# Performance work log

Measured on AMD Instinct MI355X. Metric: run time of the kernel, lower is better.

Reference implementation:

```python
import math
import jax, jax.numpy as jnp
import numpy as np

DIM = 1024
N_HEADS = 16
HEAD_DIM = DIM // N_HEADS
MAX_SEQ_LEN = 4096
ROPE_BASE = 10000.0


def _rope_tables(seq_len):
    # [S, head_dim//2] cos/sin tables, matching RotaryPositionalEncoding buffers
    inv_freq = 1.0 / (ROPE_BASE ** (jnp.arange(0, HEAD_DIM, 2, dtype=jnp.float32) / HEAD_DIM))
    t = jnp.arange(seq_len, dtype=jnp.float32)
    freqs = jnp.outer(t, inv_freq)
    return jnp.cos(freqs), jnp.sin(freqs)


def _rotate_half(x):
    # interleaved rotate: out[..., 0::2] = -x[..., 1::2]; out[..., 1::2] = x[..., 0::2]
    x1 = x[..., 0::2]
    x2 = x[..., 1::2]
    return jnp.stack([-x2, x1], axis=-1).reshape(x.shape)


def _apply_rope(xq, xk, cos, sin):
    # cos/sin: [S, head_dim//2] -> repeat_interleave(2) -> [1, 1, S, head_dim]
    cos = jnp.repeat(cos, 2, axis=-1)[None, None]
    sin = jnp.repeat(sin, 2, axis=-1)[None, None]
    xq_out = xq * cos + _rotate_half(xq) * sin
    xk_out = xk * cos + _rotate_half(xk) * sin
    return xq_out, xk_out


def setup_inputs() -> dict:
    key = jax.random.key(0)
    kx, kq, kk, kv, ko = jax.random.split(key, 5)
    B, S = 1, 4096
    x = jax.random.normal(kx, (B, S, DIM), dtype=jnp.float32)
    scale = 0.02
    Wq = jax.random.normal(kq, (DIM, DIM), dtype=jnp.float32) * scale
    Wk = jax.random.normal(kk, (DIM, DIM), dtype=jnp.float32) * scale
    Wv = jax.random.normal(kv, (DIM, DIM), dtype=jnp.float32) * scale
    Wo = jax.random.normal(ko, (DIM, DIM), dtype=jnp.float32) * scale
    return {"x": x, "Wq": Wq, "Wk": Wk, "Wv": Wv, "Wo": Wo}


def reference(x, Wq, Wk, Wv, Wo):
    B, S, _ = x.shape
    # torch nn.Linear: y = x @ W.T
    q = (x @ Wq.T).reshape(B, S, N_HEADS, HEAD_DIM).transpose(0, 2, 1, 3)  # [B,H,S,D]
    k = (x @ Wk.T).reshape(B, S, N_HEADS, HEAD_DIM).transpose(0, 2, 1, 3)
    v = (x @ Wv.T).reshape(B, S, N_HEADS, HEAD_DIM).transpose(0, 2, 1, 3)

    cos, sin = _rope_tables(S)  # start_pos = 0
    q, k = _apply_rope(q, k, cos, sin)

    scores = jnp.einsum('bhqd,bhkd->bhqk', q, k) / math.sqrt(HEAD_DIM)
    # causal mask (start_pos=0, no KV cache): upper triangle above diag gets -inf
    mask = jnp.triu(jnp.full((S, S), -jnp.inf, dtype=scores.dtype), k=1)
    scores = scores + mask[None, None]
    probs = jax.nn.softmax(scores, axis=-1)
    out = jnp.einsum('bhqk,bhkd->bhqd', probs, v)  # [B,H,S,D]
    out = out.transpose(0, 2, 1, 3).reshape(B, S, DIM)
    return out @ Wo.T
```

## Files before the change

### kernel.cpp

```cpp
#include <hip/hip_runtime.h>


typedef __attribute__((ext_vector_type(4))) float f32x4;
typedef __attribute__((ext_vector_type(8))) short short8;
typedef __attribute__((ext_vector_type(2))) unsigned int u32x2;
typedef unsigned short u16;

#define SEQ 4096
#define DIMM 1024
#define NH 16
#define HD 64

__device__ __forceinline__ u16 f2b(float f) {
  unsigned u = __float_as_uint(f);
  u += 0x7FFFu + ((u >> 16) & 1u);
  return (u16)(u >> 16);
}
__device__ __forceinline__ f32x4 mfma16(short8 a, short8 b, f32x4 c) {
  return __builtin_amdgcn_mfma_f32_16x16x32_bf16(a, b, c, 0, 0, 0);
}
#define GLL16(gp, lp)                                                        \
  __builtin_amdgcn_global_load_lds(                                          \
      (const __attribute__((address_space(1))) unsigned int*)(gp),           \
      (__attribute__((address_space(3))) unsigned int*)(lp), 16, 0, 0)

__global__ __launch_bounds__(256) void cvt_all(
    const float* __restrict__ x, const float* __restrict__ wq,
    const float* __restrict__ wk, const float* __restrict__ wv,
    const float* __restrict__ wo,
    u16* __restrict__ xb, u16* __restrict__ wqb, u16* __restrict__ wkb,
    u16* __restrict__ wvb, u16* __restrict__ wob, float2* __restrict__ tab) {
  int i = blockIdx.x * 256 + threadIdx.x;
  if (i < 2097152) {
    const float* src;
    u16* dst;
    int j;
    if (i < 1048576) {
      src = x; dst = xb; j = i;
    } else {
      int t = i - 1048576;
      int wsel = t >> 18;
      j = t & 262143;
      src = (wsel == 0) ? wq : (wsel == 1) ? wk : (wsel == 2) ? wv : wo;
      dst = (wsel == 0) ? wqb : (wsel == 1) ? wkb : (wsel == 2) ? wvb : wob;
    }
    float4 v = ((const float4*)src)[j];
    ushort4 o;
    o.x = f2b(v.x); o.y = f2b(v.y); o.z = f2b(v.z); o.w = f2b(v.w);
    ((ushort4*)dst)[j] = o;
  } else {
    int j = i - 2097152;
    int s = j >> 6, d = j & 63, fi = d >> 1;
    float ang = (float)s * powf(10000.0f, -(float)fi * (1.0f / 32.0f));
    float sn, cs;
    sincosf(ang, &sn, &cs);
    tab[j] = make_float2(cs, (d & 1) ? sn : -sn);
  }
}

template <int MODE>
__global__ __launch_bounds__(256) void gemm_bt(
    const u16* __restrict__ A, const u16* __restrict__ B, float* __restrict__ C,
    const float2* __restrict__ tab, u16* __restrict__ Qh, u16* __restrict__ Kh,
    u16* __restrict__ Vh, int K, int N) {
  __shared__ __align__(16) u16 As[2][4096];
  __shared__ __align__(16) u16 Bs[2][4096];
  const int tid = threadIdx.x;
  const int bm = blockIdx.x, bn = blockIdx.y;
  const int w = tid >> 6, lane = tid & 63;
  const int wm = w >> 1, wn = w & 1;
  const int l15 = lane & 15, g = lane >> 4;

  f32x4 acc[4][4] = {};

  const u16* Ap0 = A + (size_t)(bm * 128 + (tid >> 2)) * K + (tid & 3) * 8;
  const u16* Ap1 = Ap0 + (size_t)64 * K;
  const u16* Bp0 = B + (size_t)(bn * 128 + (tid >> 2)) * K + (tid & 3) * 8;
  const u16* Bp1 = Bp0 + (size_t)64 * K;

  GLL16(Ap0, &As[0][w * 512]);
  GLL16(Ap1, &As[0][2048 + w * 512]);
  GLL16(Bp0, &Bs[0][w * 512]);
  GLL16(Bp1, &Bs[0][2048 + w * 512]);
  __syncthreads();

  const int nk = K >> 5;
  for (int t = 0; t < nk; ++t) {
    const int cur = t & 1;
    if (t + 1 < nk) {
      const int k1 = (t + 1) * 32;
      GLL16(Ap0 + k1, &As[cur ^ 1][w * 512]);
      GLL16(Ap1 + k1, &As[cur ^ 1][2048 + w * 512]);
      GLL16(Bp0 + k1, &Bs[cur ^ 1][w * 512]);
      GLL16(Bp1 + k1, &Bs[cur ^ 1][2048 + w * 512]);
    }
    short8 af[4], bf[4];
#pragma unroll
    for (int m = 0; m < 4; ++m)
      af[m] = *(const short8*)&As[cur][(wm * 64 + m * 16 + l15) * 32 + g * 8];
#pragma unroll
    for (int n = 0; n < 4; ++n)
      bf[n] = *(const short8*)&Bs[cur][(wn * 64 + n * 16 + l15) * 32 + g * 8];
#pragma unroll
    for (int m = 0; m < 4; ++m)
#pragma unroll
      for (int n = 0; n < 4; ++n)
        acc[m][n] = mfma16(af[m], bf[n], acc[m][n]);
    __syncthreads();
  }

  if (MODE == 0) {
#pragma unroll
    for (int m = 0; m < 4; ++m) {
      int grow = bm * 128 + wm * 64 + m * 16 + g * 4;
#pragma unroll
      for (int n = 0; n < 4; ++n) {
        int gcol = bn * 128 + wn * 64 + n * 16 + l15;
#pragma unroll
        for (int r = 0; r < 4; ++r)
          C[(size_t)(grow + r) * N + gcol] = acc[m][n][r];
      }
    }
  } else {
    const int sector = bn >> 3;
    const int hh = (bn & 7) * 2 + wn;
    u16* dst = (sector == 0) ? Qh : (sector == 1) ? Kh : Vh;
    const float qs = (sector == 0) ? 0.125f : 1.0f;
#pragma unroll
    for (int m = 0; m < 4; ++m) {
#pragma unroll
      for (int n = 0; n < 4; ++n) {
        const int d = n * 16 + l15;
#pragma unroll
        for (int r = 0; r < 4; ++r) {
          const int srow = bm * 128 + wm * 64 + m * 16 + g * 4 + r;
          float v = acc[m][n][r];
          float val;
          if (sector < 2) {
            float p = __shfl_xor(v, 1);
            float2 tc = tab[srow * 64 + d];
            val = (v * tc.x + p * tc.y) * qs;
          } else {
            val = v;
          }
          float valn = __shfl_xor(val, 1);
          if (!(l15 & 1)) {
            unsigned pk;
            asm("v_cvt_pk_bf16_f32 %0, %1, %2" : "=v"(pk) : "v"(val), "v"(valn));
            *(unsigned*)&dst[((size_t)hh * SEQ + srow) * HD + d] = pk;
          }
        }
      }
    }
  }
}

__global__ __launch_bounds__(256, 4) void attn_fwd(
    const u16* __restrict__ Qh, const u16* __restrict__ Kh,
    const u16* __restrict__ Vh, u16* __restrict__ Ob) {
  __shared__ __align__(16) u16 Ks[2][64 * 64];
  __shared__ __align__(16) u16 Vt[2][64 * 64];
  __shared__ __align__(16) u16 Ps[4][16 * 64];

  const int L = blockIdx.x;
  const int xcd = L & 7, sl = L >> 3;
  const int h = xcd + 8 * (sl >> 6);
  const int cp = sl & 63;
  const int c = (cp < 32) ? (63 - 2 * cp) : (2 * (cp - 32));

  const int tid = threadIdx.x, w = tid >> 6, lane = tid & 63;
  const int l15 = lane & 15, g = lane >> 4;
  const int qr0 = c * 64 + w * 16;
  const size_t hS = (size_t)h * SEQ;

  const int krow0 = w * 8 + (lane >> 3);
  const int kc0 = ((lane & 7) ^ (krow0 & 7)) * 8;
  const int krow1 = 32 + krow0;
  const int kc1 = ((lane & 7) ^ (krow1 & 7)) * 8;
  const int kvp = tid >> 3, d0 = (tid & 7) * 8;
  const u16* Vsrc = Vh + (hS + kvp * 2) * HD + d0;
  int voff[8];
#pragma unroll
  for (int j = 0; j < 8; ++j) {
    int d = d0 + j;
    int sw = (d ^ (d >> 3)) & 7;
    voff[j] = d * 64 + (((kvp >> 2) ^ sw) << 3) + (kvp & 3) * 2;
  }

  const u16* Qp = Qh + (hS + qr0 + l15) * HD + g * 8;
  short8 qf0 = *(const short8*)(Qp);
  short8 qf1 = *(const short8*)(Qp + 32);

  f32x4 o[4] = {};
  float m_ = -3.0e38f, lg = 0.f;

  GLL16(Kh + (hS + krow0) * HD + kc0, &Ks[0][w * 512]);
  GLL16(Kh + (hS + krow1) * HD + kc1, &Ks[0][2048 + w * 512]);
  short8 va = *(const short8*)(Vsrc);
  short8 vb = *(const short8*)(Vsrc + HD);

  for (int t = 0; t <= c; ++t) {
    const int cur = t & 1;
    {
      u16* vtb = &Vt[cur][0];
#pragma unroll
      for (int j = 0; j < 8; ++j) {
        ushort2 pr;
        pr.x = (u16)va[j];
        pr.y = (u16)vb[j];
        *(ushort2*)(vtb + voff[j]) = pr;
      }
    }
    __syncthreads();
    if (t < c) {
      const size_t kb_ = hS + (size_t)(t + 1) * 64;
      GLL16(Kh + (kb_ + krow0) * HD + kc0, &Ks[cur ^ 1][w * 512]);
      GLL16(Kh + (kb_ + krow1) * HD + kc1, &Ks[cur ^ 1][2048 + w * 512]);
      va = *(const short8*)(Vsrc + (size_t)(t + 1) * 64 * HD);
      vb = *(const short8*)(Vsrc + (size_t)(t + 1) * 64 * HD + HD);
    }
    f32x4 s[4] = {};
#pragma unroll
    for (int kb = 0; kb < 4; ++kb) {
      int row = kb * 16 + l15;
      short8 k0 = *(const short8*)&Ks[cur][row * 64 + ((g ^ (row & 7)) << 3)];
      short8 k1 = *(const short8*)&Ks[cur][row * 64 + (((4 + g) ^ (row & 7)) << 3)];
      s[kb] = mfma16(k0, qf0, s[kb]);
      s[kb] = mfma16(k1, qf1, s[kb]);
    }
    if (t == c) {
      const int kv0 = t * 64;
      int q = qr0 + l15;
#pragma unroll
      for (int kb = 0; kb < 4; ++kb) {
        int kvb = kv0 + kb * 16 + g * 4;
#pragma unroll
        for (int r = 0; r < 4; ++r)
          if (kvb + r > q) s[kb][r] = -1.0e30f;
      }
    }
    float mx = fmaxf(fmaxf(fmaxf(s[0][0], s[0][1]), fmaxf(s[0][2], s[0][3])),
                     fmaxf(fmaxf(fmaxf(s[1][0], s[1][1]), fmaxf(s[1][2], s[1][3])),
                           fmaxf(fmaxf(fmaxf(s[2][0], s[2][1]), fmaxf(s[2][2], s[2][3])),
                                 fmaxf(fmaxf(s[3][0], s[3][1]), fmaxf(s[3][2], s[3][3])))));
    mx = fmaxf(mx, __shfl_xor(mx, 16));
    mx = fmaxf(mx, __shfl_xor(mx, 32));
    if (!__all(mx - m_ <= 8.0f)) {
      float nm = fmaxf(m_, mx);
      float sc = __expf(m_ - nm);
      m_ = nm;
      lg *= sc;
#pragma unroll
      for (int r = 0; r < 4; ++r) {
        float so = __shfl(sc, g * 4 + r);
        o[0][r] *= so; o[1][r] *= so; o[2][r] *= so; o[3][r] *= so;
      }
    }
    {
      float ps = 0.f;
#pragma unroll
      for (int kb = 0; kb < 4; ++kb) {
        float p0 = __expf(s[kb][0] - m_);
        float p1 = __expf(s[kb][1] - m_);
        float p2 = __expf(s[kb][2] - m_);
        float p3 = __expf(s[kb][3] - m_);
        ps += (p0 + p1) + (p2 + p3);
        unsigned w0, w1;
        asm("v_cvt_pk_bf16_f32 %0, %1, %2" : "=v"(w0) : "v"(p0), "v"(p1));
        asm("v_cvt_pk_bf16_f32 %0, %1, %2" : "=v"(w1) : "v"(p2), "v"(p3));
        int ch = (kb * 2 + (g >> 1)) ^ (l15 & 7);
        *(u32x2*)&Ps[w][l15 * 64 + ch * 8 + (g & 1) * 4] = (u32x2){w0, w1};
      }
      lg += ps;
    }
    short8 pa0 = *(const short8*)&Ps[w][l15 * 64 + ((g ^ (l15 & 7)) << 3)];
    short8 pa1 = *(const short8*)&Ps[w][l15 * 64 + (((4 + g) ^ (l15 & 7)) << 3)];
#pragma unroll
    for (int nb = 0; nb < 4; ++nb) {
      int rv = nb * 16 + l15;
      int swv = (rv ^ (rv >> 3)) & 7;
      short8 v0f = *(const short8*)&Vt[cur][rv * 64 + ((g ^ swv) << 3)];
      short8 v1f = *(const short8*)&Vt[cur][rv * 64 + (((4 + g) ^ swv) << 3)];
      o[nb] = mfma16(pa0, v0f, o[nb]);
      o[nb] = mfma16(pa1, v1f, o[nb]);
    }
  }

  float l = lg;
  l += __shfl_xor(l, 16);
  l += __shfl_xor(l, 32);
  float il = 1.0f / l;
#pragma unroll
  for (int r = 0; r < 4; ++r) {
    float ilr = __shfl(il, g * 4 + r);
    int qrow = qr0 + g * 4 + r;
#pragma unroll
    for (int nb = 0; nb < 4; ++nb)
      Ob[(size_t)qrow * DIMM + h * HD + nb * 16 + l15] = f2b(o[nb][r] * ilr);
  }
}

#define OFF_XB 0u
#define OFF_WQKV 8388608u
#define OFF_WOB 14680064u
#define OFF_TAB 16777216u
#define OFF_QH 18874368u
#define OFF_KH 27262976u
#define OFF_VH 35651584u
#define OFF_OB 44040192u

extern "C" void kernel_launch(void* const* d_in, const int* in_sizes, int n_in,
                              void* d_out, int out_size, void* d_ws, size_t ws_size,
                              hipStream_t stream) {
  const float* x = (const float*)d_in[0];
  const float* Wq = (const float*)d_in[1];
  const float* Wk = (const float*)d_in[2];
  const float* Wv = (const float*)d_in[3];
  const float* Wo = (const float*)d_in[4];
  float* out = (float*)d_out;
  char* ws = (char*)d_ws;

  u16* xb = (u16*)(ws + OFF_XB);
  u16* wqkv = (u16*)(ws + OFF_WQKV);
  u16* wqb = wqkv;
  u16* wkb = wqkv + (size_t)DIMM * DIMM;
  u16* wvb = wqkv + (size_t)2 * DIMM * DIMM;
  u16* wob = (u16*)(ws + OFF_WOB);
  float2* tab = (float2*)(ws + OFF_TAB);
  u16* Qh = (u16*)(ws + OFF_QH);
  u16* Kh = (u16*)(ws + OFF_KH);
  u16* Vh = (u16*)(ws + OFF_VH);
  u16* Ob = (u16*)(ws + OFF_OB);

  cvt_all<<<9216, 256, 0, stream>>>(x, Wq, Wk, Wv, Wo, xb, wqb, wkb, wvb, wob, tab);

  gemm_bt<1><<<dim3(SEQ / 128, 3072 / 128), 256, 0, stream>>>(
      xb, wqkv, nullptr, tab, Qh, Kh, Vh, DIMM, 3072);

  attn_fwd<<<1024, 256, 0, stream>>>(Qh, Kh, Vh, Ob);

  gemm_bt<0><<<dim3(SEQ / 128, DIMM / 128), 256, 0, stream>>>(
      Ob, wob, out, nullptr, nullptr, nullptr, nullptr, DIMM, DIMM);
}
```

Baseline: 257.9 us.

## Triple-buffer GEMM loads, simplify attention block mapping, raise MFMA priority

The GEMM moves from a double- to a triple-buffered LDS pipeline with two tiles in flight. It uses explicit vmcnt waits and a single barrier per iteration instead of two __syncthreads. The attention kernel drops the XCD-aware head/chunk interleaving for a simple longest-first mapping. It also wraps the QK and PV MFMA sections in s_setprio to favour matrix work across waves. Triple buffering raises GEMM LDS use, which may reduce occupancy, and the new block order may lose L2 locality per XCD.

```diff
diff --git a/kernel.cpp b/kernel.cpp
--- a/kernel.cpp
+++ b/kernel.cpp
@@ -63,8 +63,8 @@
     const u16* __restrict__ A, const u16* __restrict__ B, float* __restrict__ C,
     const float2* __restrict__ tab, u16* __restrict__ Qh, u16* __restrict__ Kh,
     u16* __restrict__ Vh, int K, int N) {
-  __shared__ __align__(16) u16 As[2][4096];
-  __shared__ __align__(16) u16 Bs[2][4096];
+  __shared__ __align__(16) u16 As[3][4096];
+  __shared__ __align__(16) u16 Bs[3][4096];
   const int tid = threadIdx.x;
   const int bm = blockIdx.x, bn = blockIdx.y;
   const int w = tid >> 6, lane = tid & 63;
@@ -82,17 +82,27 @@
   GLL16(Ap1, &As[0][2048 + w * 512]);
   GLL16(Bp0, &Bs[0][w * 512]);
   GLL16(Bp1, &Bs[0][2048 + w * 512]);
-  __syncthreads();
+  GLL16(Ap0 + 32, &As[1][w * 512]);
+  GLL16(Ap1 + 32, &As[1][2048 + w * 512]);
+  GLL16(Bp0 + 32, &Bs[1][w * 512]);
+  GLL16(Bp1 + 32, &Bs[1][2048 + w * 512]);
 
   const int nk = K >> 5;
+  int cur = 0;
   for (int t = 0; t < nk; ++t) {
-    const int cur = t & 1;
-    if (t + 1 < nk) {
-      const int k1 = (t + 1) * 32;
-      GLL16(Ap0 + k1, &As[cur ^ 1][w * 512]);
-      GLL16(Ap1 + k1, &As[cur ^ 1][2048 + w * 512]);
-      GLL16(Bp0 + k1, &Bs[cur ^ 1][w * 512]);
-      GLL16(Bp1 + k1, &Bs[cur ^ 1][2048 + w * 512]);
+    if (t + 1 < nk)
+      asm volatile("s_waitcnt vmcnt(4)" ::: "memory");
+    else
+      asm volatile("s_waitcnt vmcnt(0)" ::: "memory");
+    __builtin_amdgcn_s_barrier();
+    asm volatile("" ::: "memory");
+    if (t + 2 < nk) {
+      const int k2 = (t + 2) * 32;
+      const int nb = (t + 2) % 3;
+      GLL16(Ap0 + k2, &As[nb][w * 512]);
+      GLL16(Ap1 + k2, &As[nb][2048 + w * 512]);
+      GLL16(Bp0 + k2, &Bs[nb][w * 512]);
+      GLL16(Bp1 + k2, &Bs[nb][2048 + w * 512]);
     }
     short8 af[4], bf[4];
 #pragma unroll
@@ -106,7 +116,7 @@
 #pragma unroll
       for (int n = 0; n < 4; ++n)
         acc[m][n] = mfma16(af[m], bf[n], acc[m][n]);
-    __syncthreads();
+    cur = (cur == 2) ? 0 : cur + 1;
   }
 
   if (MODE == 0) {
@@ -163,10 +173,8 @@
   __shared__ __align__(16) u16 Ps[4][16 * 64];
 
   const int L = blockIdx.x;
-  const int xcd = L & 7, sl = L >> 3;
-  const int h = xcd + 8 * (sl >> 6);
-  const int cp = sl & 63;
-  const int c = (cp < 32) ? (63 - 2 * cp) : (2 * (cp - 32));
+  const int h = L & 15;
+  const int c = 63 - (L >> 4);
 
   const int tid = threadIdx.x, w = tid >> 6, lane = tid & 63;
   const int l15 = lane & 15, g = lane >> 4;
@@ -220,6 +228,7 @@
       vb = *(const short8*)(Vsrc + (size_t)(t + 1) * 64 * HD + HD);
     }
     f32x4 s[4] = {};
+    __builtin_amdgcn_s_setprio(1);
 #pragma unroll
     for (int kb = 0; kb < 4; ++kb) {
       int row = kb * 16 + l15;
@@ -228,6 +237,7 @@
       s[kb] = mfma16(k0, qf0, s[kb]);
       s[kb] = mfma16(k1, qf1, s[kb]);
     }
+    __builtin_amdgcn_s_setprio(0);
     if (t == c) {
       const int kv0 = t * 64;
       int q = qr0 + l15;
@@ -275,6 +285,7 @@
     }
     short8 pa0 = *(const short8*)&Ps[w][l15 * 64 + ((g ^ (l15 & 7)) << 3)];
     short8 pa1 = *(const short8*)&Ps[w][l15 * 64 + (((4 + g) ^ (l15 & 7)) << 3)];
+    __builtin_amdgcn_s_setprio(1);
 #pragma unroll
     for (int nb = 0; nb < 4; ++nb) {
       int rv = nb * 16 + l15;
@@ -284,6 +295,7 @@
       o[nb] = mfma16(pa0, v0f, o[nb]);
       o[nb] = mfma16(pa1, v1f, o[nb]);
     }
+    __builtin_amdgcn_s_setprio(0);
   }
 
   float l = lg;
```

Result: no change. 257.2 us (-0.3%).

## Split long causal attention rows across two blocks and merge partials

Applied to the files above, without the earlier changes.

Query tiles whose causal range is 32 or more KV tiles are now split into two halves processed by separate blocks. Each half writes unnormalized fp32 partial outputs plus its running max and sum, and a new merge kernel combines them. The change also narrows the output projection tile to 128x64 for more blocks, adds setprio around the MFMA sections, and packs the QKV epilogue stores so every lane writes. The aim is to cut load imbalance and the long tail from the heaviest causal tiles, at the cost of an extra kernel launch and added fp32 partial traffic.

```diff
diff --git a/kernel.cpp b/kernel.cpp
--- a/kernel.cpp
+++ b/kernel.cpp
@@ -58,11 +58,11 @@
   }
 }
 
-template <int MODE>
-__global__ __launch_bounds__(256) void gemm_bt(
-    const u16* __restrict__ A, const u16* __restrict__ B, float* __restrict__ C,
+__global__ __launch_bounds__(256) void gemm_qkv(
+    const u16* __restrict__ A, const u16* __restrict__ B,
     const float2* __restrict__ tab, u16* __restrict__ Qh, u16* __restrict__ Kh,
-    u16* __restrict__ Vh, int K, int N) {
+    u16* __restrict__ Vh) {
+  const int K = DIMM;
   __shared__ __align__(16) u16 As[2][4096];
   __shared__ __align__(16) u16 Bs[2][4096];
   const int tid = threadIdx.x;
@@ -109,64 +109,136 @@
     __syncthreads();
   }
 
-  if (MODE == 0) {
-#pragma unroll
-    for (int m = 0; m < 4; ++m) {
-      int grow = bm * 128 + wm * 64 + m * 16 + g * 4;
-#pragma unroll
-      for (int n = 0; n < 4; ++n) {
-        int gcol = bn * 128 + wn * 64 + n * 16 + l15;
-#pragma unroll
-        for (int r = 0; r < 4; ++r)
-          C[(size_t)(grow + r) * N + gcol] = acc[m][n][r];
-      }
-    }
-  } else {
-    const int sector = bn >> 3;
-    const int hh = (bn & 7) * 2 + wn;
-    u16* dst = (sector == 0) ? Qh : (sector == 1) ? Kh : Vh;
-    const float qs = (sector == 0) ? 0.125f : 1.0f;
-#pragma unroll
-    for (int m = 0; m < 4; ++m) {
-#pragma unroll
-      for (int n = 0; n < 4; ++n) {
-        const int d = n * 16 + l15;
-#pragma unroll
-        for (int r = 0; r < 4; ++r) {
-          const int srow = bm * 128 + wm * 64 + m * 16 + g * 4 + r;
-          float v = acc[m][n][r];
-          float val;
-          if (sector < 2) {
-            float p = __shfl_xor(v, 1);
-            float2 tc = tab[srow * 64 + d];
-            val = (v * tc.x + p * tc.y) * qs;
-          } else {
-            val = v;
-          }
-          float valn = __shfl_xor(val, 1);
-          if (!(l15 & 1)) {
-            unsigned pk;
-            asm("v_cvt_pk_bf16_f32 %0, %1, %2" : "=v"(pk) : "v"(val), "v"(valn));
-            *(unsigned*)&dst[((size_t)hh * SEQ + srow) * HD + d] = pk;
-          }
+  const int sector = bn >> 3;
+  const int hh = (bn & 7) * 2 + wn;
+  u16* dst = (sector == 0) ? Qh : (sector == 1) ? Kh : Vh;
+  const float qs = (sector == 0) ? 0.125f : 1.0f;
+  const int evenlane = !(l15 & 1);
+  const int dd0 = (l15 & ~1);
+#pragma unroll
+  for (int m = 0; m < 4; ++m) {
+    const int sb = bm * 128 + wm * 64 + m * 16 + g * 4;
+#pragma unroll
+    for (int n = 0; n < 4; ++n) {
+      const int d = n * 16 + l15;
+      float val[4];
+#pragma unroll
+      for (int r = 0; r < 4; ++r) {
+        float v = acc[m][n][r];
+        if (sector < 2) {
+          float p = __shfl_xor(v, 1);
+          float2 tc = tab[(sb + r) * 64 + d];
+          val[r] = (v * tc.x + p * tc.y) * qs;
+        } else {
+          val[r] = v;
         }
       }
+      float x0 = __shfl_xor(val[0], 1);
+      float x1 = __shfl_xor(val[1], 1);
+      float x2 = __shfl_xor(val[2], 1);
+      float x3 = __shfl_xor(val[3], 1);
+      float aLo = evenlane ? val[0] : x2;
+      float aHi = evenlane ? x0 : val[2];
+      float bLo = evenlane ? val[1] : x3;
+      float bHi = evenlane ? x1 : val[3];
+      unsigned pkA, pkB;
+      asm("v_cvt_pk_bf16_f32 %0, %1, %2" : "=v"(pkA) : "v"(aLo), "v"(aHi));
+      asm("v_cvt_pk_bf16_f32 %0, %1, %2" : "=v"(pkB) : "v"(bLo), "v"(bHi));
+      const int rA = evenlane ? 0 : 2, rB = evenlane ? 1 : 3;
+      const int dcol = n * 16 + dd0;
+      *(unsigned*)&dst[((size_t)hh * SEQ + sb + rA) * HD + dcol] = pkA;
+      *(unsigned*)&dst[((size_t)hh * SEQ + sb + rB) * HD + dcol] = pkB;
+    }
+  }
+}
+
+__global__ __launch_bounds__(256) void gemm_o(
+    const u16* __restrict__ A, const u16* __restrict__ B, float* __restrict__ C) {
+  const int K = DIMM;
+  __shared__ __align__(16) u16 As[2][4096];
+  __shared__ __align__(16) u16 Bs[2][2048];
+  const int tid = threadIdx.x;
+  const int bm = blockIdx.x, bn = blockIdx.y;
+  const int w = tid >> 6, lane = tid & 63;
+  const int wm = w >> 1, wn = w & 1;
+  const int l15 = lane & 15, g = lane >> 4;
+
+  f32x4 acc[4][2] = {};
+
+  const u16* Ap0 = A + (size_t)(bm * 128 + (tid >> 2)) * K + (tid & 3) * 8;
+  const u16* Ap1 = Ap0 + (size_t)64 * K;
+  const u16* Bp0 = B + (size_t)(bn * 64 + (tid >> 2)) * K + (tid & 3) * 8;
+
+  GLL16(Ap0, &As[0][w * 512]);
+  GLL16(Ap1, &As[0][2048 + w * 512]);
+  GLL16(Bp0, &Bs[0][w * 512]);
+  __syncthreads();
+
+  const int nk = K >> 5;
+  for (int t = 0; t < nk; ++t) {
+    const int cur = t & 1;
+    if (t + 1 < nk) {
+      const int k1 = (t + 1) * 32;
+      GLL16(Ap0 + k1, &As[cur ^ 1][w * 512]);
+      GLL16(Ap1 + k1, &As[cur ^ 1][2048 + w * 512]);
+      GLL16(Bp0 + k1, &Bs[cur ^ 1][w * 512]);
+    }
+    short8 af[4], bf[2];
+#pragma unroll
+    for (int m = 0; m < 4; ++m)
+      af[m] = *(const short8*)&As[cur][(wm * 64 + m * 16 + l15) * 32 + g * 8];
+#pragma unroll
+    for (int n = 0; n < 2; ++n)
+      bf[n] = *(const short8*)&Bs[cur][(wn * 32 + n * 16 + l15) * 32 + g * 8];
+#pragma unroll
+    for (int m = 0; m < 4; ++m)
+#pragma unroll
+      for (int n = 0; n < 2; ++n)
+        acc[m][n] = mfma16(af[m], bf[n], acc[m][n]);
+    __syncthreads();
+  }
+
+#pragma unroll
+  for (int m = 0; m < 4; ++m) {
+    int grow = bm * 128 + wm * 64 + m * 16 + g * 4;
+#pragma unroll
+    for (int n = 0; n < 2; ++n) {
+      int gcol = bn * 64 + wn * 32 + n * 16 + l15;
+#pragma unroll
+      for (int r = 0; r < 4; ++r)
+        C[(size_t)(grow + r) * DIMM + gcol] = acc[m][n][r];
     }
   }
 }
 
 __global__ __launch_bounds__(256, 4) void attn_fwd(
     const u16* __restrict__ Qh, const u16* __restrict__ Kh,
-    const u16* __restrict__ Vh, u16* __restrict__ Ob) {
+    const u16* __restrict__ Vh, u16* __restrict__ Ob,
+    float* __restrict__ Opart, float2* __restrict__ ml) {
   __shared__ __align__(16) u16 Ks[2][64 * 64];
   __shared__ __align__(16) u16 Vt[2][64 * 64];
   __shared__ __align__(16) u16 Ps[4][16 * 64];
 
   const int L = blockIdx.x;
-  const int xcd = L & 7, sl = L >> 3;
-  const int h = xcd + 8 * (sl >> 6);
-  const int cp = sl & 63;
-  const int c = (cp < 32) ? (63 - 2 * cp) : (2 * (cp - 32));
+  const int h = L & 15;
+  const int u = L >> 4;
+  int c, t0, t1, half = 0;
+  if (u < 80) {
+    int i = u / 5, j = u % 5;
+    if (j < 4) {
+      c = 63 - 2 * i - (j >> 1);
+      half = j & 1;
+      int mid = (c + 2) >> 1;
+      t0 = half ? mid : 0;
+      t1 = half ? (c + 1) : mid;
+    } else {
+      c = 31 - i; t0 = 0; t1 = c + 1;
+    }
+  } else {
+    c = 15 - (u - 80); t0 = 0; t1 = c + 1;
+  }
+  const int heavy = (c >= 32);
+  const int nt = t1 - t0;
 
   const int tid = threadIdx.x, w = tid >> 6, lane = tid & 63;
   const int l15 = lane & 15, g = lane >> 4;
@@ -194,13 +266,14 @@
   f32x4 o[4] = {};
   float m_ = -3.0e38f, lg = 0.f;
 
-  GLL16(Kh + (hS + krow0) * HD + kc0, &Ks[0][w * 512]);
-  GLL16(Kh + (hS + krow1) * HD + kc1, &Ks[0][2048 + w * 512]);
-  short8 va = *(const short8*)(Vsrc);
-  short8 vb = *(const short8*)(Vsrc + HD);
-
-  for (int t = 0; t <= c; ++t) {
-    const int cur = t & 1;
+  GLL16(Kh + (hS + (size_t)t0 * 64 + krow0) * HD + kc0, &Ks[0][w * 512]);
+  GLL16(Kh + (hS + (size_t)t0 * 64 + krow1) * HD + kc1, &Ks[0][2048 + w * 512]);
+  short8 va = *(const short8*)(Vsrc + (size_t)t0 * 64 * HD);
+  short8 vb = *(const short8*)(Vsrc + (size_t)t0 * 64 * HD + HD);
+
+  for (int tt = 0; tt < nt; ++tt) {
+    const int t = t0 + tt;
+    const int cur = tt & 1;
     {
       u16* vtb = &Vt[cur][0];
 #pragma unroll
@@ -212,7 +285,7 @@
       }
     }
     __syncthreads();
-    if (t < c) {
+    if (tt + 1 < nt) {
       const size_t kb_ = hS + (size_t)(t + 1) * 64;
       GLL16(Kh + (kb_ + krow0) * HD + kc0, &Ks[cur ^ 1][w * 512]);
       GLL16(Kh + (kb_ + krow1) * HD + kc1, &Ks[cur ^ 1][2048 + w * 512]);
@@ -220,6 +293,7 @@
       vb = *(const short8*)(Vsrc + (size_t)(t + 1) * 64 * HD + HD);
     }
     f32x4 s[4] = {};
+    __builtin_amdgcn_s_setprio(1);
 #pragma unroll
     for (int kb = 0; kb < 4; ++kb) {
       int row = kb * 16 + l15;
@@ -228,6 +302,7 @@
       s[kb] = mfma16(k0, qf0, s[kb]);
       s[kb] = mfma16(k1, qf1, s[kb]);
     }
+    __builtin_amdgcn_s_setprio(0);
     if (t == c) {
       const int kv0 = t * 64;
       int q = qr0 + l15;
@@ -275,6 +350,7 @@
     }
     short8 pa0 = *(const short8*)&Ps[w][l15 * 64 + ((g ^ (l15 & 7)) << 3)];
     short8 pa1 = *(const short8*)&Ps[w][l15 * 64 + (((4 + g) ^ (l15 & 7)) << 3)];
+    __builtin_amdgcn_s_setprio(1);
 #pragma unroll
     for (int nb = 0; nb < 4; ++nb) {
       int rv = nb * 16 + l15;
@@ -284,19 +360,61 @@
       o[nb] = mfma16(pa0, v0f, o[nb]);
       o[nb] = mfma16(pa1, v1f, o[nb]);
     }
+    __builtin_amdgcn_s_setprio(0);
   }
 
   float l = lg;
   l += __shfl_xor(l, 16);
   l += __shfl_xor(l, 32);
-  float il = 1.0f / l;
-#pragma unroll
-  for (int r = 0; r < 4; ++r) {
-    float ilr = __shfl(il, g * 4 + r);
-    int qrow = qr0 + g * 4 + r;
+  if (heavy) {
+    const int p = (h * 32 + (c - 32)) * 2 + half;
+    if (lane < 16)
+      ml[p * 64 + w * 16 + l15] = make_float2(m_, l);
+    float* Od = Opart + ((size_t)p << 12);
 #pragma unroll
     for (int nb = 0; nb < 4; ++nb)
-      Ob[(size_t)qrow * DIMM + h * HD + nb * 16 + l15] = f2b(o[nb][r] * ilr);
+#pragma unroll
+      for (int r = 0; r < 4; ++r)
+        Od[(w * 16 + g * 4 + r) * 64 + nb * 16 + l15] = o[nb][r];
+  } else {
+    float il = 1.0f / l;
+#pragma unroll
+    for (int r = 0; r < 4; ++r) {
+      float ilr = __shfl(il, g * 4 + r);
+      int qrow = qr0 + g * 4 + r;
+#pragma unroll
+      for (int nb = 0; nb < 4; ++nb)
+        Ob[(size_t)qrow * DIMM + h * HD + nb * 16 + l15] = f2b(o[nb][r] * ilr);
+    }
+  }
+}
+
+__global__ __launch_bounds__(256) void attn_merge(
+    const float* __restrict__ Opart, const float2* __restrict__ ml,
+    u16* __restrict__ Ob) {
+  const int slot = blockIdx.x;
+  const int h = slot >> 5;
+  const int c = 32 + (slot & 31);
+  const int t = threadIdx.x;
+  const int q = t >> 2, dq = (t & 3) << 4;
+  const int pA = slot * 2, pB = pA + 1;
+  float2 a = ml[pA * 64 + q], b = ml[pB * 64 + q];
+  float m = fmaxf(a.x, b.x);
+  float fA = __expf(a.x - m), fB = __expf(b.x - m);
+  float il = 1.0f / (a.y * fA + b.y * fB);
+  const float* OA = Opart + ((size_t)pA << 12) + q * 64 + dq;
+  const float* OB = Opart + ((size_t)pB << 12) + q * 64 + dq;
+  u16* dst = Ob + (size_t)(c * 64 + q) * DIMM + h * HD + dq;
+#pragma unroll
+  for (int jj = 0; jj < 16; jj += 4) {
+    float4 va = *(const float4*)(OA + jj);
+    float4 vb = *(const float4*)(OB + jj);
+    ushort4 o4;
+    o4.x = f2b((va.x * fA + vb.x * fB) * il);
+    o4.y = f2b((va.y * fA + vb.y * fB) * il);
+    o4.z = f2b((va.z * fA + vb.z * fB) * il);
+    o4.w = f2b((va.w * fA + vb.w * fB) * il);
+    *(ushort4*)(dst + jj) = o4;
   }
 }
 
@@ -308,6 +426,8 @@
 #define OFF_KH 27262976u
 #define OFF_VH 35651584u
 #define OFF_OB 44040192u
+#define OFF_OPART 52428800u
+#define OFF_ML 69206016u
 
 extern "C" void kernel_launch(void* const* d_in, const int* in_sizes, int n_in,
                               void* d_out, int out_size, void* d_ws, size_t ws_size,
@@ -331,14 +451,16 @@
   u16* Kh = (u16*)(ws + OFF_KH);
   u16* Vh = (u16*)(ws + OFF_VH);
   u16* Ob = (u16*)(ws + OFF_OB);
+  float* Opart = (float*)(ws + OFF_OPART);
+  float2* ml = (float2*)(ws + OFF_ML);
 
   cvt_all<<<9216, 256, 0, stream>>>(x, Wq, Wk, Wv, Wo, xb, wqb, wkb, wvb, wob, tab);
 
-  gemm_bt<1><<<dim3(SEQ / 128, 3072 / 128), 256, 0, stream>>>(
-      xb, wqkv, nullptr, tab, Qh, Kh, Vh, DIMM, 3072);
-
-  attn_fwd<<<1024, 256, 0, stream>>>(Qh, Kh, Vh, Ob);
-
-  gemm_bt<0><<<dim3(SEQ / 128, DIMM / 128), 256, 0, stream>>>(
-      Ob, wob, out, nullptr, nullptr, nullptr, nullptr, DIMM, DIMM);
-}
+  gemm_qkv<<<dim3(32, 24), 256, 0, stream>>>(xb, wqkv, tab, Qh, Kh, Vh);
+
+  attn_fwd<<<1536, 256, 0, stream>>>(Qh, Kh, Vh, Ob, Opart, ml);
+
+  attn_merge<<<512, 256, 0, stream>>>(Opart, ml, Ob);
+
+  gemm_o<<<dim3(32, 16), 256, 0, stream>>>(Ob, wob, out);
+}
```

Measured after the change: 231.0 us. 1.12x faster.
